# Kernel optimization log

Hardware: AMD Instinct MI355X
Metric: run time of the kernel (lower is better)

## Reference

```python
import jax, jax.numpy as jnp
import numpy as np

NHEAD, HD, ITERS = 8, 32, 6


def _layernorm(x, g, b, eps=1e-5):
    mu = jnp.mean(x, axis=-1, keepdims=True)
    var = jnp.mean((x - mu) ** 2, axis=-1, keepdims=True)
    return g * (x - mu) / jnp.sqrt(var + eps) + b


def _msa1(x, ax, WQ, bQ, WK, bK, WV, bV, WO, bO):
    # ring (sliding-window, size 3) attention + relay node as 4th key/value
    B, L, H = x.shape
    q = (x @ WQ + bQ).reshape(B, L, NHEAD, HD)
    k = (x @ WK + bK).reshape(B, L, NHEAD, HD)
    ak = (ax @ WK + bK).reshape(B, 1, NHEAD, 1, HD)   # relay key
    av = (ax @ WV + bV).reshape(B, 1, NHEAD, 1, HD)   # relay value
    padk = jnp.pad(k, ((0, 0), (1, 1), (0, 0), (0, 0)))
    wins = jnp.stack([padk[:, t:L + t] for t in range(3)], axis=3)  # [B,L,nh,3,hd]
    ak_b = jnp.broadcast_to(ak, (B, L, NHEAD, 1, HD))
    av_b = jnp.broadcast_to(av, (B, L, NHEAD, 1, HD))
    keys = jnp.concatenate([ak_b, wins], axis=3)   # [B,L,nh,4,hd]
    # NOTE: faithful to source bug: window VALUES come from k (pad_v = F.pad(k,...))
    vals = jnp.concatenate([av_b, wins], axis=3)
    scores = jnp.einsum('blnd,blnkd->blnk', q, keys) / np.sqrt(HD).astype(np.float32)
    alphas = jax.nn.softmax(scores, axis=-1)
    att = jnp.einsum('blnk,blnkd->blnd', alphas, vals).reshape(B, L, NHEAD * HD)
    return att @ WO + bO


def _msa2(x, y, WQ, bQ, WK, bK, WV, bV, WO, bO):
    # relay attends over [relay; nodes]; mask arg is ignored in the original
    B, L1, H = y.shape
    q = (x @ WQ + bQ).reshape(B, NHEAD, HD)
    k = (y @ WK + bK).reshape(B, L1, NHEAD, HD)
    v = (y @ WV + bV).reshape(B, L1, NHEAD, HD)
    scores = jnp.einsum('bnd,blnd->bnl', q, k) / np.sqrt(HD).astype(np.float32)
    alphas = jax.nn.softmax(scores, axis=-1)
    att = jnp.einsum('bnl,blnd->bnd', alphas, v).reshape(B, NHEAD * HD)
    return att @ WO + bO


def setup_inputs() -> dict:
    key = jax.random.key(0)
    ks = jax.random.split(key, 32)
    B, L, H, V, E, I = 32, 512, 256, 32000, 300, 6

    def rn(k, shape, s=0.05):
        return jax.random.normal(k, shape, jnp.float32) * s

    inp = {
        'data': jax.random.randint(ks[0], (B, L), 0, V),
        'emb': rn(ks[1], (V, E), 0.1),
        'emb_fc_W': rn(ks[2], (E, H)),
        'emb_fc_b': jnp.zeros((H,), jnp.float32),
        'pos_emb': rn(ks[3], (1000, H), 0.02),
        'ln_g': jnp.ones((I, H), jnp.float32),
        'ln_b': jnp.zeros((I, H), jnp.float32),
    }
    names = ['r_WQ', 'r_WK', 'r_WV', 'r_WO', 's_WQ', 's_WK', 's_WV', 's_WO']
    for j, n in enumerate(names):
        inp[n] = rn(ks[4 + j], (I, H, H))
        inp[n.replace('W', 'b')] = rn(ks[12 + j], (I, H), 0.01)
    return inp


def reference(data, emb, emb_fc_W, emb_fc_b, pos_emb, ln_g, ln_b,
              r_WQ, r_bQ, r_WK, r_bK, r_WV, r_bV, r_WO, r_bO,
              s_WQ, s_bQ, s_WK, s_bK, s_WV, s_bV, s_WO, s_bO):
    B, L = data.shape
    mask = (data == 1)
    e = emb[data]                                  # [B,L,nemb]
    P = pos_emb[:L][None]                          # [1,L,H]
    x0 = e @ emb_fc_W + emb_fc_b + P               # [B,L,H]
    nodes = x0
    relay = jnp.mean(x0, axis=1)                   # [B,H]
    for i in range(ITERS):
        ax = relay
        n_ln = _layernorm(nodes, ln_g[i], ln_b[i])
        nodes = nodes + jax.nn.leaky_relu(
            _msa1(n_ln, ax, r_WQ[i], r_bQ[i], r_WK[i], r_bK[i],
                  r_WV[i], r_bV[i], r_WO[i], r_bO[i]))
        y = jnp.concatenate([relay[:, None, :], nodes], axis=1)
        relay = jax.nn.leaky_relu(
            _msa2(relay, y, s_WQ[i], s_bQ[i], s_WK[i], s_bK[i],
                  s_WV[i], s_bV[i], s_WO[i], s_bO[i]))
        nodes = jnp.where(mask[:, :, None], 0.0, nodes)
    rep = 0.5 * jnp.max(nodes, axis=1) + 0.5 * relay
    return rep
```

## Files before the change

### kernel.cpp

```cpp
#include <hip/hip_runtime.h>
#include <stdint.h>

typedef __bf16 bf16x8 __attribute__((ext_vector_type(8)));
typedef unsigned short ushort8 __attribute__((ext_vector_type(8)));
typedef float floatx4 __attribute__((ext_vector_type(4)));

__device__ __forceinline__ unsigned short f2b(float f) {
    unsigned int u = __builtin_bit_cast(unsigned int, f);
    u += 0x7fffu + ((u >> 16) & 1u);
    return (unsigned short)(u >> 16);
}
__device__ __forceinline__ float b2f(unsigned short u) {
    union { unsigned int i; float f; } x; x.i = ((unsigned int)u) << 16; return x.f;
}
__device__ __forceinline__ void gl_lds16(const unsigned short* g, unsigned short* l) {
    __builtin_amdgcn_global_load_lds(
        (const __attribute__((address_space(1))) unsigned int*)g,
        (__attribute__((address_space(3))) unsigned int*)l, 16, 0, 0);
}

#define SCALE_QK 0.17677669529663687f

__global__ __launch_bounds__(256) void transpose_many(const float* __restrict__ w0,
                                                      const float* __restrict__ w1,
                                                      const float* __restrict__ w2,
                                                      const float* __restrict__ w3,
                                                      const float* __restrict__ w4,
                                                      unsigned short* __restrict__ out) {
    __shared__ float tile[64][65];
    int m = blockIdx.y;
    int fam = m / 6, it = m % 6;
    const float* src =
        (fam == 0 ? w0 : fam == 1 ? w1 : fam == 2 ? w2 : fam == 3 ? w3 : w4) + it * 65536;
    unsigned short* dst = out + (size_t)(it * 5 + fam) * 65536;
    int k0 = (blockIdx.x & 3) * 64, n0 = (blockIdx.x >> 2) * 64;
    int tid = threadIdx.x;
    int rg = tid >> 6, cl = tid & 63;
#pragma unroll
    for (int i = 0; i < 16; i++) {
        int kl = rg * 16 + i;
        tile[kl][cl] = src[(k0 + kl) * 256 + n0 + cl];
    }
    __syncthreads();
#pragma unroll
    for (int i = 0; i < 16; i++) {
        int nl = rg * 16 + i;
        dst[(n0 + nl) * 256 + k0 + cl] = f2b(tile[cl][nl]);
    }
}

__global__ void transpose_emb(const float* __restrict__ W,
                              unsigned short* __restrict__ out) {
    int e = blockIdx.x * 256 + threadIdx.x;
    int n = e / 320, k = e % 320;
    out[e] = (k < 300) ? f2b(W[k * 256 + n]) : (unsigned short)0;
}

__global__ void gather_emb(const int* __restrict__ data,
                           const float* __restrict__ emb,
                           unsigned short* __restrict__ apad) {
    int row = blockIdx.x;
    int tok = data[row];
    const float* er = emb + (size_t)tok * 300;
    for (int c = threadIdx.x; c < 320; c += 256)
        apad[(size_t)row * 320 + c] = (c < 300) ? f2b(er[c]) : (unsigned short)0;
}

template <int EPI, int KDIM>
__global__ __launch_bounds__(256) void gemm_k(const unsigned short* __restrict__ A,
                                              const unsigned short* __restrict__ Bt,
                                              const float* __restrict__ bias0,
                                              const float* __restrict__ bias1,
                                              float* __restrict__ outF,
                                              unsigned short* __restrict__ outB0,
                                              unsigned short* __restrict__ outB1,
                                              const float* __restrict__ pos,
                                              const int* __restrict__ dmask,
                                              int applyMask) {
    constexpr int G = KDIM / 8;
    __shared__ unsigned short Asm[64 * KDIM];
    __shared__ unsigned short Bsm[64 * KDIM];
    const int tid = threadIdx.x;
    const int wave = tid >> 6, lane = tid & 63;
    const int wm = (wave >> 1) * 32, wn = (wave & 1) * 32;
    const int quad = lane >> 4, l16 = lane & 15;
    const int rowBase = blockIdx.x * 64, colBase = blockIdx.y * 64;
    {
        const unsigned short* gbA = A + (size_t)(rowBase + wave * 16) * KDIM;
        const unsigned short* gbB = Bt + (size_t)(colBase + wave * 16) * KDIM;
        unsigned short* lbA = Asm + wave * 16 * KDIM;
        unsigned short* lbB = Bsm + wave * 16 * KDIM;
#pragma unroll
        for (int c = 0; c < G / 4; c++) {
            int gi = c * 64 + lane;
            int rl = gi / G, sl = gi - rl * G;
            int sg = sl ^ (rl & 7);
            gl_lds16(gbA + rl * KDIM + sg * 8, lbA + gi * 8);
            gl_lds16(gbB + rl * KDIM + sg * 8, lbB + gi * 8);
        }
    }
    __syncthreads();

    floatx4 acc[2][2] = {};
    const int mr0 = wm + l16, mr1 = wm + 16 + l16;
    const int nr0 = wn + l16, nr1 = wn + 16 + l16;
#pragma unroll
    for (int ks = 0; ks < KDIM / 32; ks++) {
        int g = ks * 4 + quad;
        bf16x8 af0 = __builtin_bit_cast(bf16x8, *(const ushort8*)&Asm[mr0 * KDIM + ((g ^ (mr0 & 7)) * 8)]);
        bf16x8 af1 = __builtin_bit_cast(bf16x8, *(const ushort8*)&Asm[mr1 * KDIM + ((g ^ (mr1 & 7)) * 8)]);
        bf16x8 bf0 = __builtin_bit_cast(bf16x8, *(const ushort8*)&Bsm[nr0 * KDIM + ((g ^ (nr0 & 7)) * 8)]);
        bf16x8 bf1 = __builtin_bit_cast(bf16x8, *(const ushort8*)&Bsm[nr1 * KDIM + ((g ^ (nr1 & 7)) * 8)]);
        acc[0][0] = __builtin_amdgcn_mfma_f32_16x16x32_bf16(af0, bf0, acc[0][0], 0, 0, 0);
        acc[0][1] = __builtin_amdgcn_mfma_f32_16x16x32_bf16(af0, bf1, acc[0][1], 0, 0, 0);
        acc[1][0] = __builtin_amdgcn_mfma_f32_16x16x32_bf16(af1, bf0, acc[1][0], 0, 0, 0);
        acc[1][1] = __builtin_amdgcn_mfma_f32_16x16x32_bf16(af1, bf1, acc[1][1], 0, 0, 0);
    }
    if (EPI == 0) {
        const int group = colBase >> 8;
        const float* bias = group ? bias1 : bias0;
        unsigned short* obf = group ? outB1 : outB0;
        unsigned short* tile = Asm;
        __syncthreads();
#pragma unroll
        for (int tm = 0; tm < 2; tm++) {
#pragma unroll
            for (int tn = 0; tn < 2; tn++) {
                int lcl = wn + tn * 16 + l16;
                float bv = bias[(colBase & 255) + lcl];
#pragma unroll
                for (int r = 0; r < 4; r++) {
                    int rl = wm + tm * 16 + quad * 4 + r;
                    tile[rl * 72 + lcl] = f2b(acc[tm][tn][r] + bv);
                }
            }
        }
        __syncthreads();
#pragma unroll
        for (int j = 0; j < 2; j++) {
            int c = j * 256 + tid;
            int rl = c >> 3, c8 = c & 7;
            ushort8 v = *(const ushort8*)&tile[rl * 72 + c8 * 8];
            *(ushort8*)(obf + (size_t)(rowBase + rl) * 256 + (colBase & 255) + c8 * 8) = v;
        }
    } else {
#pragma unroll
        for (int tm = 0; tm < 2; tm++) {
#pragma unroll
            for (int tn = 0; tn < 2; tn++) {
                int col = colBase + wn + tn * 16 + l16;
                int lc = col & 255;
                float bv = bias0[lc];
#pragma unroll
                for (int r = 0; r < 4; r++) {
                    int row = rowBase + wm + tm * 16 + quad * 4 + r;
                    float c = acc[tm][tn][r] + bv;
                    size_t o = (size_t)row * 256 + lc;
                    if (EPI == 1) {
                        float v = c > 0.f ? c : 0.01f * c;
                        float base = outF[o];
                        if (applyMask && dmask[row] == 1) base = 0.f;
                        float rr = base + v;
                        outF[o] = rr;
                        outB0[o] = f2b(rr);
                    } else {
                        outF[o] = c + pos[(row & 511) * 256 + lc];
                    }
                }
            }
        }
    }
}

__global__ void mean_part(const float* __restrict__ nodes, float* __restrict__ part) {
    int b = blockIdx.x, c = blockIdx.y, h = threadIdx.x;
    const float* p = nodes + ((size_t)b * 512 + c * 32) * 256 + h;
    float s = 0.f;
    for (int l = 0; l < 32; l++) s += p[l * 256];
    part[(b * 16 + c) * 256 + h] = s;
}
__global__ void mean_comb(const float* __restrict__ part, float* __restrict__ relay) {
    int b = blockIdx.x, h = threadIdx.x;
    float s = 0.f;
    for (int c = 0; c < 16; c++) s += part[(b * 16 + c) * 256 + h];
    relay[b * 256 + h] = s * (1.f / 512.f);
}

__global__ __launch_bounds__(256) void ln_k(const float* __restrict__ nodes,
                                            const float* __restrict__ g,
                                            const float* __restrict__ bb,
                                            unsigned short* __restrict__ out,
                                            const int* __restrict__ dmask,
                                            int applyMask) {
    __shared__ float red[8];
    int row = blockIdx.x, t = threadIdx.x;
    int wv = t >> 6, ln_ = t & 63;
    float x = nodes[(size_t)row * 256 + t];
    if (applyMask && dmask[row] == 1) x = 0.f;
    float s = x;
#pragma unroll
    for (int o = 32; o; o >>= 1) s += __shfl_xor(s, o);
    if (ln_ == 0) red[wv] = s;
    __syncthreads();
    float mu = (red[0] + red[1] + red[2] + red[3]) * (1.f / 256.f);
    float d = x - mu;
    float v = d * d;
#pragma unroll
    for (int o = 32; o; o >>= 1) v += __shfl_xor(v, o);
    if (ln_ == 0) red[4 + wv] = v;
    __syncthreads();
    float var = (red[4] + red[5] + red[6] + red[7]) * (1.f / 256.f);
    float inv = rsqrtf(var + 1e-5f);
    out[(size_t)row * 256 + t] = f2b(g[t] * d * inv + bb[t]);
}

__global__ __launch_bounds__(1024) void relay5(const float* __restrict__ relay,
                       const float* __restrict__ rWK, const float* __restrict__ rbK,
                       const float* __restrict__ rWV, const float* __restrict__ rbV,
                       const float* __restrict__ sWQ, const float* __restrict__ sbQ,
                       const float* __restrict__ sWK, const float* __restrict__ sbK,
                       const float* __restrict__ sWV, const float* __restrict__ sbV,
                       float* __restrict__ AK, float* __restrict__ AV,
                       float* __restrict__ Q2, float* __restrict__ RK2, float* __restrict__ RV2) {
    __shared__ float r[256];
    __shared__ float part[1024];
    int b = blockIdx.x, fam = blockIdx.y, t = threadIdx.x;
    if (t < 256) r[t] = relay[b * 256 + t];
    __syncthreads();
    const float* W; const float* bi; float* o;
    switch (fam) {
        case 0: W = rWK; bi = rbK; o = AK; break;
        case 1: W = rWV; bi = rbV; o = AV; break;
        case 2: W = sWQ; bi = sbQ; o = Q2; break;
        case 3: W = sWK; bi = sbK; o = RK2; break;
        default: W = sWV; bi = sbV; o = RV2; break;
    }
    int col = t & 255, kc = t >> 8;
    float s = 0.f;
    for (int e = kc * 64; e < kc * 64 + 64; e++) s += r[e] * W[e * 256 + col];
    part[t] = s;
    __syncthreads();
    if (kc == 0)
        o[b * 256 + col] = part[col] + part[256 + col] + part[512 + col] + part[768 + col] + bi[col];
}

__global__ __launch_bounds__(256) void attn1_k(const unsigned short* __restrict__ q,
                                               const unsigned short* __restrict__ k,
                                               const float* __restrict__ ak,
                                               const float* __restrict__ av,
                                               unsigned short* __restrict__ att) {
    int tid = threadIdx.x;
    int row = blockIdx.x * 4 + (tid >> 6);
    int b = row >> 9, l = row & 511;
    int t = tid & 63;
    size_t o = (size_t)row * 256 + t * 4;
    ushort4 z4; z4.x = z4.y = z4.z = z4.w = 0;
    ushort4 q4 = *(const ushort4*)(q + o);
    ushort4 k04 = *(const ushort4*)(k + o);
    ushort4 km4 = (l > 0) ? *(const ushort4*)(k + o - 256) : z4;
    ushort4 kp4 = (l < 511) ? *(const ushort4*)(k + o + 256) : z4;
    float4 akv = *(const float4*)(ak + b * 256 + t * 4);
    float4 avv = *(const float4*)(av + b * 256 + t * 4);
    float qv0 = b2f(q4.x), qv1 = b2f(q4.y), qv2 = b2f(q4.z), qv3 = b2f(q4.w);
    float k00 = b2f(k04.x), k01 = b2f(k04.y), k02 = b2f(k04.z), k03 = b2f(k04.w);
    float km0 = b2f(km4.x), km1 = b2f(km4.y), km2 = b2f(km4.z), km3 = b2f(km4.w);
    float kp0 = b2f(kp4.x), kp1 = b2f(kp4.y), kp2 = b2f(kp4.z), kp3 = b2f(kp4.w);
    float s0 = qv0 * akv.x + qv1 * akv.y + qv2 * akv.z + qv3 * akv.w;
    float s1 = qv0 * km0 + qv1 * km1 + qv2 * km2 + qv3 * km3;
    float s2 = qv0 * k00 + qv1 * k01 + qv2 * k02 + qv3 * k03;
    float s3 = qv0 * kp0 + qv1 * kp1 + qv2 * kp2 + qv3 * kp3;
#pragma unroll
    for (int off = 4; off; off >>= 1) {
        s0 += __shfl_xor(s0, off);
        s1 += __shfl_xor(s1, off);
        s2 += __shfl_xor(s2, off);
        s3 += __shfl_xor(s3, off);
    }
    s0 *= SCALE_QK; s1 *= SCALE_QK; s2 *= SCALE_QK; s3 *= SCALE_QK;
    float m = fmaxf(fmaxf(s0, s1), fmaxf(s2, s3));
    float e0 = __expf(s0 - m), e1 = __expf(s1 - m), e2 = __expf(s2 - m), e3 = __expf(s3 - m);
    float iZ = 1.f / (e0 + e1 + e2 + e3);
    ushort4 r4;
    r4.x = f2b((e0 * avv.x + e1 * km0 + e2 * k00 + e3 * kp0) * iZ);
    r4.y = f2b((e0 * avv.y + e1 * km1 + e2 * k01 + e3 * kp1) * iZ);
    r4.z = f2b((e0 * avv.z + e1 * km2 + e2 * k02 + e3 * kp2) * iZ);
    r4.w = f2b((e0 * avv.w + e1 * km3 + e2 * k03 + e3 * kp3) * iZ);
    *(ushort4*)(att + o) = r4;
}

__global__ __launch_bounds__(512) void attn2_k(const float* __restrict__ q2,
                                               const unsigned short* __restrict__ k2,
                                               const unsigned short* __restrict__ v2,
                                               const float* __restrict__ rk2,
                                               const float* __restrict__ rv2,
                                               float* __restrict__ att2) {
    __shared__ float sc[513];
    __shared__ float qs[32];
    __shared__ float red[16];
    __shared__ float red2[512];
    int bn = blockIdx.x;
    int b = bn >> 3, n = bn & 7;
    int t = threadIdx.x;
    if (t < 32) qs[t] = q2[b * 256 + n * 32 + t];
    __syncthreads();
    float lmax = -1e30f;
    for (int li = t; li < 513; li += 512) {
        float d = 0.f;
        if (li == 0) {
            const float* kr = rk2 + b * 256 + n * 32;
#pragma unroll 8
            for (int j = 0; j < 32; j++) d += qs[j] * kr[j];
        } else {
            const unsigned short* kr = k2 + ((size_t)(b * 512 + li - 1) * 256 + n * 32);
#pragma unroll 8
            for (int j = 0; j < 32; j++) d += qs[j] * b2f(kr[j]);
        }
        d *= SCALE_QK;
        sc[li] = d;
        lmax = fmaxf(lmax, d);
    }
#pragma unroll
    for (int o = 32; o; o >>= 1) lmax = fmaxf(lmax, __shfl_xor(lmax, o));
    if ((t & 63) == 0) red[t >> 6] = lmax;
    __syncthreads();
    float m = red[0];
#pragma unroll
    for (int i = 1; i < 8; i++) m = fmaxf(m, red[i]);
    float lsum = 0.f;
    for (int li = t; li < 513; li += 512) {
        float e = __expf(sc[li] - m);
        sc[li] = e;
        lsum += e;
    }
#pragma unroll
    for (int o = 32; o; o >>= 1) lsum += __shfl_xor(lsum, o);
    if ((t & 63) == 0) red[8 + (t >> 6)] = lsum;
    __syncthreads();
    float Z = red[8];
#pragma unroll
    for (int i = 9; i < 16; i++) Z += red[i];
    int d_ = t & 31, g_ = t >> 5;
    float acc = 0.f;
    for (int li = g_; li < 513; li += 16) {
        if (li == 0) {
            acc += sc[0] * rv2[b * 256 + n * 32 + d_];
        } else {
            acc += sc[li] * b2f(v2[(size_t)(b * 512 + li - 1) * 256 + n * 32 + d_]);
        }
    }
    red2[t] = acc;
    __syncthreads();
    if (t < 32) {
        float s = 0.f;
#pragma unroll
        for (int g = 0; g < 16; g++) s += red2[g * 32 + t];
        att2[b * 256 + n * 32 + t] = s / Z;
    }
}

__global__ __launch_bounds__(1024) void relay_out2(const float* __restrict__ att2,
                           const float* __restrict__ WO, const float* __restrict__ bO,
                           float* __restrict__ relay) {
    __shared__ float r[256];
    __shared__ float part[1024];
    int b = blockIdx.x, t = threadIdx.x;
    if (t < 256) r[t] = att2[b * 256 + t];
    __syncthreads();
    int col = t & 255, kc = t >> 8;
    float s = 0.f;
    for (int e = kc * 64; e < kc * 64 + 64; e++) s += r[e] * WO[e * 256 + col];
    part[t] = s;
    __syncthreads();
    if (kc == 0) {
        float tot = part[col] + part[256 + col] + part[512 + col] + part[768 + col] + bO[col];
        relay[b * 256 + col] = tot > 0.f ? tot : 0.01f * tot;
    }
}

__global__ void rep_part(const float* __restrict__ nodes, const int* __restrict__ dmask,
                         float* __restrict__ part) {
    int b = blockIdx.x, c = blockIdx.y, h = threadIdx.x;
    const float* p = nodes + ((size_t)b * 512 + c * 32) * 256 + h;
    const int* dd = dmask + b * 512 + c * 32;
    float m = -1e30f;
    for (int l = 0; l < 32; l++) {
        float v = (dd[l] == 1) ? 0.f : p[l * 256];
        m = fmaxf(m, v);
    }
    part[(b * 16 + c) * 256 + h] = m;
}
__global__ void rep_comb(const float* __restrict__ part, const float* __restrict__ relay,
                         float* __restrict__ out) {
    int b = blockIdx.x, h = threadIdx.x;
    float m = -1e30f;
    for (int c = 0; c < 16; c++) m = fmaxf(m, part[(b * 16 + c) * 256 + h]);
    out[b * 256 + h] = 0.5f * m + 0.5f * relay[b * 256 + h];
}

extern "C" void kernel_launch(void* const* d_in, const int* in_sizes, int n_in,
                              void* d_out, int out_size, void* d_ws, size_t ws_size,
                              hipStream_t stream) {
    const int* data = (const int*)d_in[0];
    const float* emb = (const float*)d_in[1];
    const float* emb_fc_W = (const float*)d_in[2];
    const float* emb_fc_b = (const float*)d_in[3];
    const float* pos_emb = (const float*)d_in[4];
    const float* ln_g = (const float*)d_in[5];
    const float* ln_b = (const float*)d_in[6];
    const float* r_WQ = (const float*)d_in[7];
    const float* r_bQ = (const float*)d_in[8];
    const float* r_WK = (const float*)d_in[9];
    const float* r_bK = (const float*)d_in[10];
    const float* r_WV = (const float*)d_in[11];
    const float* r_bV = (const float*)d_in[12];
    const float* r_WO = (const float*)d_in[13];
    const float* r_bO = (const float*)d_in[14];
    const float* s_WQ = (const float*)d_in[15];
    const float* s_bQ = (const float*)d_in[16];
    const float* s_WK = (const float*)d_in[17];
    const float* s_bK = (const float*)d_in[18];
    const float* s_WV = (const float*)d_in[19];
    const float* s_bV = (const float*)d_in[20];
    const float* s_WO = (const float*)d_in[21];
    const float* s_bO = (const float*)d_in[22];

    char* w = (char*)d_ws;
    size_t off = 0;
    auto alloc = [&](size_t bytes) -> char* {
        char* p = w + off;
        off += (bytes + 255) & ~(size_t)255;
        return p;
    };
    float* RELAY = (float*)alloc(8192 * 4);
    float* AK = (float*)alloc(8192 * 4);
    float* AV = (float*)alloc(8192 * 4);
    float* Q2 = (float*)alloc(8192 * 4);
    float* RK2 = (float*)alloc(8192 * 4);
    float* RV2 = (float*)alloc(8192 * 4);
    float* ATT2 = (float*)alloc(8192 * 4);
    float* PART = (float*)alloc((size_t)32 * 16 * 256 * 4);
    unsigned short* WTE = (unsigned short*)alloc((size_t)256 * 320 * 2);
    unsigned short* WT = (unsigned short*)alloc((size_t)30 * 65536 * 2);
    float* NODES = (float*)alloc((size_t)16384 * 256 * 4);
    unsigned short* NLN = (unsigned short*)alloc((size_t)16384 * 256 * 2);
    unsigned short* Qb = (unsigned short*)alloc((size_t)16384 * 256 * 2);
    unsigned short* Kb16 = (unsigned short*)alloc((size_t)16384 * 256 * 2);
    unsigned short* NBF = (unsigned short*)alloc((size_t)16384 * 320 * 2);
    unsigned short* AEMB = NBF;
    unsigned short* ATT = NLN;
    unsigned short* K2b = Qb;
    unsigned short* V2b = Kb16;

    transpose_many<<<dim3(16, 30), 256, 0, stream>>>(r_WQ, r_WK, r_WO, s_WK, s_WV, WT);
    transpose_emb<<<320, 256, 0, stream>>>(emb_fc_W, WTE);
    gather_emb<<<16384, 256, 0, stream>>>(data, emb, AEMB);
    gemm_k<2, 320><<<dim3(256, 4), 256, 0, stream>>>(AEMB, WTE, emb_fc_b, nullptr,
                                                     NODES, nullptr, nullptr, pos_emb, nullptr, 0);
    mean_part<<<dim3(32, 16), 256, 0, stream>>>(NODES, PART);
    mean_comb<<<32, 256, 0, stream>>>(PART, RELAY);

    for (int i = 0; i < 6; i++) {
        const unsigned short* wQK = WT + (size_t)(i * 5 + 0) * 65536;
        const unsigned short* wO = WT + (size_t)(i * 5 + 2) * 65536;
        const unsigned short* wKV2 = WT + (size_t)(i * 5 + 3) * 65536;

        ln_k<<<16384, 256, 0, stream>>>(NODES, ln_g + i * 256, ln_b + i * 256, NLN, data, i > 0);
        gemm_k<0, 256><<<dim3(256, 8), 256, 0, stream>>>(NLN, wQK, r_bQ + i * 256, r_bK + i * 256,
                                                         nullptr, Qb, Kb16, nullptr, nullptr, 0);
        relay5<<<dim3(32, 5), 1024, 0, stream>>>(RELAY,
                                                r_WK + (size_t)i * 65536, r_bK + i * 256,
                                                r_WV + (size_t)i * 65536, r_bV + i * 256,
                                                s_WQ + (size_t)i * 65536, s_bQ + i * 256,
                                                s_WK + (size_t)i * 65536, s_bK + i * 256,
                                                s_WV + (size_t)i * 65536, s_bV + i * 256,
                                                AK, AV, Q2, RK2, RV2);
        attn1_k<<<4096, 256, 0, stream>>>(Qb, Kb16, AK, AV, ATT);
        gemm_k<1, 256><<<dim3(256, 4), 256, 0, stream>>>(ATT, wO, r_bO + i * 256, nullptr,
                                                         NODES, NBF, nullptr, nullptr, data, i > 0);
        gemm_k<0, 256><<<dim3(256, 8), 256, 0, stream>>>(NBF, wKV2, s_bK + i * 256, s_bV + i * 256,
                                                         nullptr, K2b, V2b, nullptr, nullptr, 0);
        attn2_k<<<256, 512, 0, stream>>>(Q2, K2b, V2b, RK2, RV2, ATT2);
        relay_out2<<<32, 1024, 0, stream>>>(ATT2, s_WO + (size_t)i * 65536, s_bO + i * 256, RELAY);
    }
    rep_part<<<dim3(32, 16), 256, 0, stream>>>(NODES, data, PART);
    rep_comb<<<32, 256, 0, stream>>>(PART, RELAY, (float*)d_out);
}
```

Measured before the change: 753.2 us.

## Fuse layernorm into QK GEMM and relay projections into relay output step

LayerNorm is folded into a new QK GEMM kernel that normalizes fp32 rows straight into swizzled LDS, so the separate LN pass and its bf16 intermediate buffer are gone. The relay output projection now also computes the five relay projections for the next iteration in one 32-block kernel, replacing the per-iteration relay5 launch. The two-stage mean and max reductions become single kernels. This cuts launches and one full activation round trip per iteration, at the cost of each GEMM block recomputing LN for its rows across 8 column tiles, and a serial 32-block relay kernel doing six matvecs.

```diff
diff --git a/kernel.cpp b/kernel.cpp
--- a/kernel.cpp
+++ b/kernel.cpp
@@ -172,46 +172,117 @@
     }
 }
 
-__global__ void mean_part(const float* __restrict__ nodes, float* __restrict__ part) {
-    int b = blockIdx.x, c = blockIdx.y, h = threadIdx.x;
-    const float* p = nodes + ((size_t)b * 512 + c * 32) * 256 + h;
+__global__ __launch_bounds__(256) void lnqk_gemm(const float* __restrict__ nodes,
+                                                 const float* __restrict__ lg,
+                                                 const float* __restrict__ lb,
+                                                 const unsigned short* __restrict__ Bt,
+                                                 const float* __restrict__ bQ,
+                                                 const float* __restrict__ bK,
+                                                 unsigned short* __restrict__ Qb,
+                                                 unsigned short* __restrict__ Kb,
+                                                 const int* __restrict__ dmask,
+                                                 int applyMask) {
+    __shared__ unsigned short Asm[64 * 256];
+    __shared__ unsigned short Bsm[64 * 256];
+    const int tid = threadIdx.x;
+    const int wave = tid >> 6, lane = tid & 63;
+    const int rowBase = blockIdx.x * 64, colBase = blockIdx.y * 64;
+    {
+        const unsigned short* gb = Bt + (size_t)(colBase + wave * 16) * 256;
+        unsigned short* lb_ = Bsm + wave * 16 * 256;
+#pragma unroll
+        for (int c = 0; c < 8; c++) {
+            int gi = c * 64 + lane;
+            int rl = gi >> 5, sl = gi & 31;
+            int sg = sl ^ (rl & 7);
+            gl_lds16(gb + rl * 256 + sg * 8, lb_ + gi * 8);
+        }
+    }
+    {
+        const int cb = lane * 4;
+        float4 gv = *(const float4*)(lg + cb);
+        float4 bv = *(const float4*)(lb + cb);
+        for (int i = 0; i < 16; i++) {
+            int row = rowBase + wave * 16 + i;
+            float4 x = *(const float4*)(nodes + (size_t)row * 256 + cb);
+            if (applyMask && dmask[row] == 1) { x.x = 0.f; x.y = 0.f; x.z = 0.f; x.w = 0.f; }
+            float s = x.x + x.y + x.z + x.w;
+            float qq = x.x * x.x + x.y * x.y + x.z * x.z + x.w * x.w;
+#pragma unroll
+            for (int o = 32; o; o >>= 1) { s += __shfl_xor(s, o); qq += __shfl_xor(qq, o); }
+            float mu = s * (1.f / 256.f);
+            float var = qq * (1.f / 256.f) - mu * mu;
+            float inv = rsqrtf(fmaxf(var, 0.f) + 1e-5f);
+            ushort4 r4;
+            r4.x = f2b(gv.x * (x.x - mu) * inv + bv.x);
+            r4.y = f2b(gv.y * (x.y - mu) * inv + bv.y);
+            r4.z = f2b(gv.z * (x.z - mu) * inv + bv.z);
+            r4.w = f2b(gv.w * (x.w - mu) * inv + bv.w);
+            int r = wave * 16 + i;
+            int slot = (lane >> 1) ^ (r & 7);
+            *(ushort4*)&Asm[r * 256 + slot * 8 + (lane & 1) * 4] = r4;
+        }
+    }
+    __syncthreads();
+
+    floatx4 acc[2][2] = {};
+    const int wm = (wave >> 1) * 32, wn = (wave & 1) * 32;
+    const int quad = lane >> 4, l16 = lane & 15;
+    const int mr0 = wm + l16, mr1 = wm + 16 + l16;
+    const int nr0 = wn + l16, nr1 = wn + 16 + l16;
+#pragma unroll
+    for (int ks = 0; ks < 8; ks++) {
+        int g = ks * 4 + quad;
+        bf16x8 af0 = __builtin_bit_cast(bf16x8, *(const ushort8*)&Asm[mr0 * 256 + ((g ^ (mr0 & 7)) * 8)]);
+        bf16x8 af1 = __builtin_bit_cast(bf16x8, *(const ushort8*)&Asm[mr1 * 256 + ((g ^ (mr1 & 7)) * 8)]);
+        bf16x8 bf0 = __builtin_bit_cast(bf16x8, *(const ushort8*)&Bsm[nr0 * 256 + ((g ^ (nr0 & 7)) * 8)]);
+        bf16x8 bf1 = __builtin_bit_cast(bf16x8, *(const ushort8*)&Bsm[nr1 * 256 + ((g ^ (nr1 & 7)) * 8)]);
+        acc[0][0] = __builtin_amdgcn_mfma_f32_16x16x32_bf16(af0, bf0, acc[0][0], 0, 0, 0);
+        acc[0][1] = __builtin_amdgcn_mfma_f32_16x16x32_bf16(af0, bf1, acc[0][1], 0, 0, 0);
+        acc[1][0] = __builtin_amdgcn_mfma_f32_16x16x32_bf16(af1, bf0, acc[1][0], 0, 0, 0);
+        acc[1][1] = __builtin_amdgcn_mfma_f32_16x16x32_bf16(af1, bf1, acc[1][1], 0, 0, 0);
+    }
+    const int group = colBase >> 8;
+    const float* bias = group ? bK : bQ;
+    unsigned short* obf = group ? Kb : Qb;
+    unsigned short* tile = Asm;
+    __syncthreads();
+#pragma unroll
+    for (int tm = 0; tm < 2; tm++) {
+#pragma unroll
+        for (int tn = 0; tn < 2; tn++) {
+            int lcl = wn + tn * 16 + l16;
+            float bv = bias[(colBase & 255) + lcl];
+#pragma unroll
+            for (int r = 0; r < 4; r++) {
+                int rl = wm + tm * 16 + quad * 4 + r;
+                tile[rl * 72 + lcl] = f2b(acc[tm][tn][r] + bv);
+            }
+        }
+    }
+    __syncthreads();
+#pragma unroll
+    for (int j = 0; j < 2; j++) {
+        int c = j * 256 + tid;
+        int rl = c >> 3, c8 = c & 7;
+        ushort8 v = *(const ushort8*)&tile[rl * 72 + c8 * 8];
+        *(ushort8*)(obf + (size_t)(rowBase + rl) * 256 + (colBase & 255) + c8 * 8) = v;
+    }
+}
+
+__global__ __launch_bounds__(1024) void mean_k(const float* __restrict__ nodes,
+                                               float* __restrict__ relay) {
+    __shared__ float part[1024];
+    int b = blockIdx.x, t = threadIdx.x;
+    int col = t & 255, rg = t >> 8;
+    const float* p = nodes + ((size_t)b * 512 + rg * 128) * 256 + col;
     float s = 0.f;
-    for (int l = 0; l < 32; l++) s += p[l * 256];
-    part[(b * 16 + c) * 256 + h] = s;
-}
-__global__ void mean_comb(const float* __restrict__ part, float* __restrict__ relay) {
-    int b = blockIdx.x, h = threadIdx.x;
-    float s = 0.f;
-    for (int c = 0; c < 16; c++) s += part[(b * 16 + c) * 256 + h];
-    relay[b * 256 + h] = s * (1.f / 512.f);
-}
-
-__global__ __launch_bounds__(256) void ln_k(const float* __restrict__ nodes,
-                                            const float* __restrict__ g,
-                                            const float* __restrict__ bb,
-                                            unsigned short* __restrict__ out,
-                                            const int* __restrict__ dmask,
-                                            int applyMask) {
-    __shared__ float red[8];
-    int row = blockIdx.x, t = threadIdx.x;
-    int wv = t >> 6, ln_ = t & 63;
-    float x = nodes[(size_t)row * 256 + t];
-    if (applyMask && dmask[row] == 1) x = 0.f;
-    float s = x;
-#pragma unroll
-    for (int o = 32; o; o >>= 1) s += __shfl_xor(s, o);
-    if (ln_ == 0) red[wv] = s;
-    __syncthreads();
-    float mu = (red[0] + red[1] + red[2] + red[3]) * (1.f / 256.f);
-    float d = x - mu;
-    float v = d * d;
-#pragma unroll
-    for (int o = 32; o; o >>= 1) v += __shfl_xor(v, o);
-    if (ln_ == 0) red[4 + wv] = v;
-    __syncthreads();
-    float var = (red[4] + red[5] + red[6] + red[7]) * (1.f / 256.f);
-    float inv = rsqrtf(var + 1e-5f);
-    out[(size_t)row * 256 + t] = f2b(g[t] * d * inv + bb[t]);
+    for (int l = 0; l < 128; l++) s += p[l * 256];
+    part[t] = s;
+    __syncthreads();
+    if (rg == 0)
+        relay[b * 256 + col] =
+            (part[col] + part[256 + col] + part[512 + col] + part[768 + col]) * (1.f / 512.f);
 }
 
 __global__ __launch_bounds__(1024) void relay5(const float* __restrict__ relay,
@@ -358,43 +429,71 @@
     }
 }
 
-__global__ __launch_bounds__(1024) void relay_out2(const float* __restrict__ att2,
-                           const float* __restrict__ WO, const float* __restrict__ bO,
-                           float* __restrict__ relay) {
+__global__ __launch_bounds__(1024) void relay_step(const float* __restrict__ att2,
+                       const float* __restrict__ WO, const float* __restrict__ bO,
+                       const float* __restrict__ rWK, const float* __restrict__ rbK,
+                       const float* __restrict__ rWV, const float* __restrict__ rbV,
+                       const float* __restrict__ sWQ, const float* __restrict__ sbQ,
+                       const float* __restrict__ sWK, const float* __restrict__ sbK,
+                       const float* __restrict__ sWV, const float* __restrict__ sbV,
+                       float* __restrict__ relay,
+                       float* __restrict__ AK, float* __restrict__ AV,
+                       float* __restrict__ Q2, float* __restrict__ RK2, float* __restrict__ RV2) {
     __shared__ float r[256];
     __shared__ float part[1024];
+    __shared__ float rs[256];
     int b = blockIdx.x, t = threadIdx.x;
+    int col = t & 255, kc = t >> 8;
     if (t < 256) r[t] = att2[b * 256 + t];
     __syncthreads();
-    int col = t & 255, kc = t >> 8;
     float s = 0.f;
     for (int e = kc * 64; e < kc * 64 + 64; e++) s += r[e] * WO[e * 256 + col];
     part[t] = s;
     __syncthreads();
     if (kc == 0) {
         float tot = part[col] + part[256 + col] + part[512 + col] + part[768 + col] + bO[col];
-        relay[b * 256 + col] = tot > 0.f ? tot : 0.01f * tot;
-    }
-}
-
-__global__ void rep_part(const float* __restrict__ nodes, const int* __restrict__ dmask,
-                         float* __restrict__ part) {
-    int b = blockIdx.x, c = blockIdx.y, h = threadIdx.x;
-    const float* p = nodes + ((size_t)b * 512 + c * 32) * 256 + h;
-    const int* dd = dmask + b * 512 + c * 32;
+        tot = tot > 0.f ? tot : 0.01f * tot;
+        rs[col] = tot;
+        relay[b * 256 + col] = tot;
+    }
+    __syncthreads();
+    const float* Ws[5] = {rWK, rWV, sWQ, sWK, sWV};
+    const float* bs[5] = {rbK, rbV, sbQ, sbK, sbV};
+    float* os[5] = {AK, AV, Q2, RK2, RV2};
+#pragma unroll
+    for (int f = 0; f < 5; f++) {
+        const float* W = Ws[f];
+        float s2 = 0.f;
+        for (int e = kc * 64; e < kc * 64 + 64; e++) s2 += rs[e] * W[e * 256 + col];
+        part[t] = s2;
+        __syncthreads();
+        if (kc == 0)
+            os[f][b * 256 + col] =
+                part[col] + part[256 + col] + part[512 + col] + part[768 + col] + bs[f][col];
+        __syncthreads();
+    }
+}
+
+__global__ __launch_bounds__(1024) void rep_k2(const float* __restrict__ nodes,
+                                               const int* __restrict__ dmask,
+                                               const float* __restrict__ relay,
+                                               float* __restrict__ out) {
+    __shared__ float part[1024];
+    int b = blockIdx.x, t = threadIdx.x;
+    int col = t & 255, rg = t >> 8;
+    const float* p = nodes + ((size_t)b * 512 + rg * 128) * 256 + col;
+    const int* dd = dmask + b * 512 + rg * 128;
     float m = -1e30f;
-    for (int l = 0; l < 32; l++) {
+    for (int l = 0; l < 128; l++) {
         float v = (dd[l] == 1) ? 0.f : p[l * 256];
         m = fmaxf(m, v);
     }
-    part[(b * 16 + c) * 256 + h] = m;
-}
-__global__ void rep_comb(const float* __restrict__ part, const float* __restrict__ relay,
-                         float* __restrict__ out) {
-    int b = blockIdx.x, h = threadIdx.x;
-    float m = -1e30f;
-    for (int c = 0; c < 16; c++) m = fmaxf(m, part[(b * 16 + c) * 256 + h]);
-    out[b * 256 + h] = 0.5f * m + 0.5f * relay[b * 256 + h];
+    part[t] = m;
+    __syncthreads();
+    if (rg == 0) {
+        float mm = fmaxf(fmaxf(part[col], part[256 + col]), fmaxf(part[512 + col], part[768 + col]));
+        out[b * 256 + col] = 0.5f * mm + 0.5f * relay[b * 256 + col];
+    }
 }
 
 extern "C" void kernel_launch(void* const* d_in, const int* in_sizes, int n_in,
@@ -438,16 +537,14 @@
     float* RK2 = (float*)alloc(8192 * 4);
     float* RV2 = (float*)alloc(8192 * 4);
     float* ATT2 = (float*)alloc(8192 * 4);
-    float* PART = (float*)alloc((size_t)32 * 16 * 256 * 4);
     unsigned short* WTE = (unsigned short*)alloc((size_t)256 * 320 * 2);
     unsigned short* WT = (unsigned short*)alloc((size_t)30 * 65536 * 2);
     float* NODES = (float*)alloc((size_t)16384 * 256 * 4);
-    unsigned short* NLN = (unsigned short*)alloc((size_t)16384 * 256 * 2);
+    unsigned short* ATT = (unsigned short*)alloc((size_t)16384 * 256 * 2);
     unsigned short* Qb = (unsigned short*)alloc((size_t)16384 * 256 * 2);
     unsigned short* Kb16 = (unsigned short*)alloc((size_t)16384 * 256 * 2);
     unsigned short* NBF = (unsigned short*)alloc((size_t)16384 * 320 * 2);
     unsigned short* AEMB = NBF;
-    unsigned short* ATT = NLN;
     unsigned short* K2b = Qb;
     unsigned short* V2b = Kb16;
 
@@ -456,32 +553,34 @@
     gather_emb<<<16384, 256, 0, stream>>>(data, emb, AEMB);
     gemm_k<2, 320><<<dim3(256, 4), 256, 0, stream>>>(AEMB, WTE, emb_fc_b, nullptr,
                                                      NODES, nullptr, nullptr, pos_emb, nullptr, 0);
-    mean_part<<<dim3(32, 16), 256, 0, stream>>>(NODES, PART);
-    mean_comb<<<32, 256, 0, stream>>>(PART, RELAY);
+    mean_k<<<32, 1024, 0, stream>>>(NODES, RELAY);
+    relay5<<<dim3(32, 5), 1024, 0, stream>>>(RELAY,
+                                             r_WK, r_bK, r_WV, r_bV,
+                                             s_WQ, s_bQ, s_WK, s_bK, s_WV, s_bV,
+                                             AK, AV, Q2, RK2, RV2);
 
     for (int i = 0; i < 6; i++) {
         const unsigned short* wQK = WT + (size_t)(i * 5 + 0) * 65536;
         const unsigned short* wO = WT + (size_t)(i * 5 + 2) * 65536;
         const unsigned short* wKV2 = WT + (size_t)(i * 5 + 3) * 65536;
-
-        ln_k<<<16384, 256, 0, stream>>>(NODES, ln_g + i * 256, ln_b + i * 256, NLN, data, i > 0);
-        gemm_k<0, 256><<<dim3(256, 8), 256, 0, stream>>>(NLN, wQK, r_bQ + i * 256, r_bK + i * 256,
-                                                         nullptr, Qb, Kb16, nullptr, nullptr, 0);
-        relay5<<<dim3(32, 5), 1024, 0, stream>>>(RELAY,
-                                                r_WK + (size_t)i * 65536, r_bK + i * 256,
-                                                r_WV + (size_t)i * 65536, r_bV + i * 256,
-                                                s_WQ + (size_t)i * 65536, s_bQ + i * 256,
-                                                s_WK + (size_t)i * 65536, s_bK + i * 256,
-                                                s_WV + (size_t)i * 65536, s_bV + i * 256,
-                                                AK, AV, Q2, RK2, RV2);
+        int nx = (i < 5) ? i + 1 : 5;
+
+        lnqk_gemm<<<dim3(256, 8), 256, 0, stream>>>(NODES, ln_g + i * 256, ln_b + i * 256,
+                                                    wQK, r_bQ + i * 256, r_bK + i * 256,
+                                                    Qb, Kb16, data, i > 0);
         attn1_k<<<4096, 256, 0, stream>>>(Qb, Kb16, AK, AV, ATT);
         gemm_k<1, 256><<<dim3(256, 4), 256, 0, stream>>>(ATT, wO, r_bO + i * 256, nullptr,
                                                          NODES, NBF, nullptr, nullptr, data, i > 0);
         gemm_k<0, 256><<<dim3(256, 8), 256, 0, stream>>>(NBF, wKV2, s_bK + i * 256, s_bV + i * 256,
                                                          nullptr, K2b, V2b, nullptr, nullptr, 0);
         attn2_k<<<256, 512, 0, stream>>>(Q2, K2b, V2b, RK2, RV2, ATT2);
-        relay_out2<<<32, 1024, 0, stream>>>(ATT2, s_WO + (size_t)i * 65536, s_bO + i * 256, RELAY);
-    }
-    rep_part<<<dim3(32, 16), 256, 0, stream>>>(NODES, data, PART);
-    rep_comb<<<32, 256, 0, stream>>>(PART, RELAY, (float*)d_out);
-}
+        relay_step<<<32, 1024, 0, stream>>>(ATT2, s_WO + (size_t)i * 65536, s_bO + i * 256,
+                                            r_WK + (size_t)nx * 65536, r_bK + nx * 256,
+                                            r_WV + (size_t)nx * 65536, r_bV + nx * 256,
+                                            s_WQ + (size_t)nx * 65536, s_bQ + nx * 256,
+                                            s_WK + (size_t)nx * 65536, s_bK + nx * 256,
+                                            s_WV + (size_t)nx * 65536, s_bV + nx * 256,
+                                            RELAY, AK, AV, Q2, RK2, RV2);
+    }
+    rep_k2<<<32, 1024, 0, stream>>>(NODES, data, RELAY, (float*)d_out);
+}
```

Result: slower. 969.4 us (+28.7%).

## Fuse relay output projection with next-iteration relay projections; merge reduction kernels

Applied to the files above, without the earlier changes.

Folds the relay output projection and the following iteration's five relay projections (K,V,Q2,K2,V2) into one per-batch kernel, so the relay5 launch inside the loop goes away. The mean and final max/relay combine each become a single 1024-thread kernel instead of a partial+combine pair. This trims launch overhead along the serial relay chain. The cost is that the projections run on only 32 blocks instead of 160, which serialises more work per block. On the last iteration the kernel computes projections that are never used.

```diff
diff --git a/kernel.cpp b/kernel.cpp
--- a/kernel.cpp
+++ b/kernel.cpp
@@ -172,20 +172,6 @@
     }
 }
 
-__global__ void mean_part(const float* __restrict__ nodes, float* __restrict__ part) {
-    int b = blockIdx.x, c = blockIdx.y, h = threadIdx.x;
-    const float* p = nodes + ((size_t)b * 512 + c * 32) * 256 + h;
-    float s = 0.f;
-    for (int l = 0; l < 32; l++) s += p[l * 256];
-    part[(b * 16 + c) * 256 + h] = s;
-}
-__global__ void mean_comb(const float* __restrict__ part, float* __restrict__ relay) {
-    int b = blockIdx.x, h = threadIdx.x;
-    float s = 0.f;
-    for (int c = 0; c < 16; c++) s += part[(b * 16 + c) * 256 + h];
-    relay[b * 256 + h] = s * (1.f / 512.f);
-}
-
 __global__ __launch_bounds__(256) void ln_k(const float* __restrict__ nodes,
                                             const float* __restrict__ g,
                                             const float* __restrict__ bb,
@@ -212,6 +198,21 @@
     float var = (red[4] + red[5] + red[6] + red[7]) * (1.f / 256.f);
     float inv = rsqrtf(var + 1e-5f);
     out[(size_t)row * 256 + t] = f2b(g[t] * d * inv + bb[t]);
+}
+
+__global__ __launch_bounds__(1024) void mean_k(const float* __restrict__ nodes,
+                                               float* __restrict__ relay) {
+    __shared__ float part[1024];
+    int b = blockIdx.x, t = threadIdx.x;
+    int col = t & 255, rg = t >> 8;
+    const float* p = nodes + ((size_t)b * 512 + rg * 128) * 256 + col;
+    float s = 0.f;
+    for (int l = 0; l < 128; l++) s += p[l * 256];
+    part[t] = s;
+    __syncthreads();
+    if (rg == 0)
+        relay[b * 256 + col] =
+            (part[col] + part[256 + col] + part[512 + col] + part[768 + col]) * (1.f / 512.f);
 }
 
 __global__ __launch_bounds__(1024) void relay5(const float* __restrict__ relay,
@@ -358,43 +359,71 @@
     }
 }
 
-__global__ __launch_bounds__(1024) void relay_out2(const float* __restrict__ att2,
-                           const float* __restrict__ WO, const float* __restrict__ bO,
-                           float* __restrict__ relay) {
+__global__ __launch_bounds__(1024) void relay_step(const float* __restrict__ att2,
+                       const float* __restrict__ WO, const float* __restrict__ bO,
+                       const float* __restrict__ rWK, const float* __restrict__ rbK,
+                       const float* __restrict__ rWV, const float* __restrict__ rbV,
+                       const float* __restrict__ sWQ, const float* __restrict__ sbQ,
+                       const float* __restrict__ sWK, const float* __restrict__ sbK,
+                       const float* __restrict__ sWV, const float* __restrict__ sbV,
+                       float* __restrict__ relay,
+                       float* __restrict__ AK, float* __restrict__ AV,
+                       float* __restrict__ Q2, float* __restrict__ RK2, float* __restrict__ RV2) {
     __shared__ float r[256];
     __shared__ float part[1024];
+    __shared__ float rs[256];
     int b = blockIdx.x, t = threadIdx.x;
+    int col = t & 255, kc = t >> 8;
     if (t < 256) r[t] = att2[b * 256 + t];
     __syncthreads();
-    int col = t & 255, kc = t >> 8;
     float s = 0.f;
     for (int e = kc * 64; e < kc * 64 + 64; e++) s += r[e] * WO[e * 256 + col];
     part[t] = s;
     __syncthreads();
     if (kc == 0) {
         float tot = part[col] + part[256 + col] + part[512 + col] + part[768 + col] + bO[col];
-        relay[b * 256 + col] = tot > 0.f ? tot : 0.01f * tot;
-    }
-}
-
-__global__ void rep_part(const float* __restrict__ nodes, const int* __restrict__ dmask,
-                         float* __restrict__ part) {
-    int b = blockIdx.x, c = blockIdx.y, h = threadIdx.x;
-    const float* p = nodes + ((size_t)b * 512 + c * 32) * 256 + h;
-    const int* dd = dmask + b * 512 + c * 32;
+        tot = tot > 0.f ? tot : 0.01f * tot;
+        rs[col] = tot;
+        relay[b * 256 + col] = tot;
+    }
+    __syncthreads();
+    const float* Ws[5] = {rWK, rWV, sWQ, sWK, sWV};
+    const float* bs[5] = {rbK, rbV, sbQ, sbK, sbV};
+    float* os[5] = {AK, AV, Q2, RK2, RV2};
+#pragma unroll
+    for (int f = 0; f < 5; f++) {
+        const float* W = Ws[f];
+        float s2 = 0.f;
+        for (int e = kc * 64; e < kc * 64 + 64; e++) s2 += rs[e] * W[e * 256 + col];
+        part[t] = s2;
+        __syncthreads();
+        if (kc == 0)
+            os[f][b * 256 + col] =
+                part[col] + part[256 + col] + part[512 + col] + part[768 + col] + bs[f][col];
+        __syncthreads();
+    }
+}
+
+__global__ __launch_bounds__(1024) void rep_k2(const float* __restrict__ nodes,
+                                               const int* __restrict__ dmask,
+                                               const float* __restrict__ relay,
+                                               float* __restrict__ out) {
+    __shared__ float part[1024];
+    int b = blockIdx.x, t = threadIdx.x;
+    int col = t & 255, rg = t >> 8;
+    const float* p = nodes + ((size_t)b * 512 + rg * 128) * 256 + col;
+    const int* dd = dmask + b * 512 + rg * 128;
     float m = -1e30f;
-    for (int l = 0; l < 32; l++) {
+    for (int l = 0; l < 128; l++) {
         float v = (dd[l] == 1) ? 0.f : p[l * 256];
         m = fmaxf(m, v);
     }
-    part[(b * 16 + c) * 256 + h] = m;
-}
-__global__ void rep_comb(const float* __restrict__ part, const float* __restrict__ relay,
-                         float* __restrict__ out) {
-    int b = blockIdx.x, h = threadIdx.x;
-    float m = -1e30f;
-    for (int c = 0; c < 16; c++) m = fmaxf(m, part[(b * 16 + c) * 256 + h]);
-    out[b * 256 + h] = 0.5f * m + 0.5f * relay[b * 256 + h];
+    part[t] = m;
+    __syncthreads();
+    if (rg == 0) {
+        float mm = fmaxf(fmaxf(part[col], part[256 + col]), fmaxf(part[512 + col], part[768 + col]));
+        out[b * 256 + col] = 0.5f * mm + 0.5f * relay[b * 256 + col];
+    }
 }
 
 extern "C" void kernel_launch(void* const* d_in, const int* in_sizes, int n_in,
@@ -438,7 +467,6 @@
     float* RK2 = (float*)alloc(8192 * 4);
     float* RV2 = (float*)alloc(8192 * 4);
     float* ATT2 = (float*)alloc(8192 * 4);
-    float* PART = (float*)alloc((size_t)32 * 16 * 256 * 4);
     unsigned short* WTE = (unsigned short*)alloc((size_t)256 * 320 * 2);
     unsigned short* WT = (unsigned short*)alloc((size_t)30 * 65536 * 2);
     float* NODES = (float*)alloc((size_t)16384 * 256 * 4);
@@ -456,32 +484,34 @@
     gather_emb<<<16384, 256, 0, stream>>>(data, emb, AEMB);
     gemm_k<2, 320><<<dim3(256, 4), 256, 0, stream>>>(AEMB, WTE, emb_fc_b, nullptr,
                                                      NODES, nullptr, nullptr, pos_emb, nullptr, 0);
-    mean_part<<<dim3(32, 16), 256, 0, stream>>>(NODES, PART);
-    mean_comb<<<32, 256, 0, stream>>>(PART, RELAY);
+    mean_k<<<32, 1024, 0, stream>>>(NODES, RELAY);
+    relay5<<<dim3(32, 5), 1024, 0, stream>>>(RELAY,
+                                             r_WK, r_bK, r_WV, r_bV,
+                                             s_WQ, s_bQ, s_WK, s_bK, s_WV, s_bV,
+                                             AK, AV, Q2, RK2, RV2);
 
     for (int i = 0; i < 6; i++) {
         const unsigned short* wQK = WT + (size_t)(i * 5 + 0) * 65536;
         const unsigned short* wO = WT + (size_t)(i * 5 + 2) * 65536;
         const unsigned short* wKV2 = WT + (size_t)(i * 5 + 3) * 65536;
+        int nx = (i < 5) ? i + 1 : 5;
 
         ln_k<<<16384, 256, 0, stream>>>(NODES, ln_g + i * 256, ln_b + i * 256, NLN, data, i > 0);
         gemm_k<0, 256><<<dim3(256, 8), 256, 0, stream>>>(NLN, wQK, r_bQ + i * 256, r_bK + i * 256,
                                                          nullptr, Qb, Kb16, nullptr, nullptr, 0);
-        relay5<<<dim3(32, 5), 1024, 0, stream>>>(RELAY,
-                                                r_WK + (size_t)i * 65536, r_bK + i * 256,
-                                                r_WV + (size_t)i * 65536, r_bV + i * 256,
-                                                s_WQ + (size_t)i * 65536, s_bQ + i * 256,
-                                                s_WK + (size_t)i * 65536, s_bK + i * 256,
-                                                s_WV + (size_t)i * 65536, s_bV + i * 256,
-                                                AK, AV, Q2, RK2, RV2);
         attn1_k<<<4096, 256, 0, stream>>>(Qb, Kb16, AK, AV, ATT);
         gemm_k<1, 256><<<dim3(256, 4), 256, 0, stream>>>(ATT, wO, r_bO + i * 256, nullptr,
                                                          NODES, NBF, nullptr, nullptr, data, i > 0);
         gemm_k<0, 256><<<dim3(256, 8), 256, 0, stream>>>(NBF, wKV2, s_bK + i * 256, s_bV + i * 256,
                                                          nullptr, K2b, V2b, nullptr, nullptr, 0);
         attn2_k<<<256, 512, 0, stream>>>(Q2, K2b, V2b, RK2, RV2, ATT2);
-        relay_out2<<<32, 1024, 0, stream>>>(ATT2, s_WO + (size_t)i * 65536, s_bO + i * 256, RELAY);
-    }
-    rep_part<<<dim3(32, 16), 256, 0, stream>>>(NODES, data, PART);
-    rep_comb<<<32, 256, 0, stream>>>(PART, RELAY, (float*)d_out);
-}
+        relay_step<<<32, 1024, 0, stream>>>(ATT2, s_WO + (size_t)i * 65536, s_bO + i * 256,
+                                            r_WK + (size_t)nx * 65536, r_bK + nx * 256,
+                                            r_WV + (size_t)nx * 65536, r_bV + nx * 256,
+                                            s_WQ + (size_t)nx * 65536, s_bQ + nx * 256,
+                                            s_WK + (size_t)nx * 65536, s_bK + nx * 256,
+                                            s_WV + (size_t)nx * 65536, s_bV + nx * 256,
+                                            RELAY, AK, AV, Q2, RK2, RV2);
+    }
+    rep_k2<<<32, 1024, 0, stream>>>(NODES, data, RELAY, (float*)d_out);
+}
```

Result: slower. 866.8 us (+15.1%).
